# Kernel optimization log

Measured on AMD Instinct MI355X. Metric: run time of the kernel, lower is better.

Reference implementation:

```python
import jax, jax.numpy as jnp
import numpy as np

B, S, V, E, H, MAX_OOVS = 32, 1024, 32000, 256, 512, 12
D2 = 2 * H + 100          # encoder feature dim after binary concat
IN = E + D2               # GRU input size


def setup_inputs() -> dict:
    key = jax.random.key(0)
    ks = jax.random.split(key, 18)
    sc = 0.02
    return {
        "input_idx": jax.random.randint(ks[0], (B,), 0, V),
        "encoded": jax.random.normal(ks[1], (B, S, 2 * H), jnp.float32),
        "encoded_idx": jax.random.randint(ks[2], (B, S), 0, V + MAX_OOVS),
        "prev_state": jax.random.normal(ks[3], (B, H), jnp.float32),
        "weighted": jax.random.normal(ks[4], (B, 1, D2), jnp.float32),
        "binary_vectors": jax.random.uniform(ks[5], (B, S, 1), jnp.float32),
        "order": 1,
        "embed_table": jax.random.normal(ks[6], (V, E), jnp.float32) * sc,
        "W_ih": jax.random.normal(ks[7], (3 * H, IN), jnp.float32) * sc,
        "b_ih": jax.random.normal(ks[8], (3 * H,), jnp.float32) * sc,
        "W_hh": jax.random.normal(ks[9], (3 * H, H), jnp.float32) * sc,
        "b_hh": jax.random.normal(ks[10], (3 * H,), jnp.float32) * sc,
        "Wo_w": jax.random.normal(ks[11], (V, H), jnp.float32) * sc,
        "Wo_b": jax.random.normal(ks[12], (V,), jnp.float32) * sc,
        "Wc_w": jax.random.normal(ks[13], (H, D2), jnp.float32) * sc,
        "Wc_b": jax.random.normal(ks[14], (H,), jnp.float32) * sc,
        "Ws_w": jax.random.normal(ks[15], (H, D2), jnp.float32) * sc,
        "Ws_b": jax.random.normal(ks[16], (H,), jnp.float32) * sc,
    }


def _gru_step(x, h, W_ih, b_ih, W_hh, b_hh):
    # torch nn.GRU single-step math
    gi = x @ W_ih.T + b_ih
    gh = h @ W_hh.T + b_hh
    i_r, i_z, i_n = jnp.split(gi, 3, axis=1)
    h_r, h_z, h_n = jnp.split(gh, 3, axis=1)
    r = jax.nn.sigmoid(i_r + h_r)
    z = jax.nn.sigmoid(i_z + h_z)
    n = jnp.tanh(i_n + r * h_n)
    return (1.0 - z) * n + z * h


def reference(input_idx, encoded, encoded_idx, prev_state, weighted,
              binary_vectors, order, embed_table, W_ih, b_ih, W_hh, b_hh,
              Wo_w, Wo_b, Wc_w, Wc_b, Ws_w, Ws_b):
    b, s = encoded.shape[0], encoded.shape[1]
    vocab = Wo_w.shape[0]
    # concat binary feature expanded to 100 channels -> (b, s, 2H+100)
    bin100 = jnp.broadcast_to(binary_vectors, (b, s, 100))
    enc = jnp.concatenate([encoded, bin100], axis=2)

    if order == 0:
        prev_state = enc[:, -1] @ Ws_w.T + Ws_b
        weighted = jnp.zeros((b, 1, enc.shape[2]), enc.dtype)

    emb = embed_table[input_idx][:, None, :]          # (b,1,E)
    x = jnp.concatenate([emb, weighted], axis=2)[:, 0]  # (b, IN)
    state = _gru_step(x, prev_state, W_ih, b_ih, W_hh, b_hh)  # (b,H)

    score_g = state @ Wo_w.T + Wo_b                   # (b, V)
    sc = jnp.tanh(enc @ Wc_w.T + Wc_b)                # (b, s, H)
    score_c = jnp.tanh(jnp.einsum('bsh,bh->bs', sc, state))
    score_c = score_c + jnp.where(encoded_idx == 0, -1000.0, 0.0).astype(score_c.dtype)

    probs = jax.nn.softmax(jnp.concatenate([score_g, score_c], axis=1), axis=1)
    prob_g = probs[:, :vocab]
    prob_c = probs[:, vocab:]
    prob_c_given = prob_c / jnp.sum(prob_c)           # faithful: scalar sum over all elems

    oovs = jnp.full((b, MAX_OOVS), 1e-4, probs.dtype)
    prob_g = jnp.concatenate([prob_g, oovs], axis=1)  # (b, V+OOV)

    # scatter-add copy probs into vocab space (same math as one_hot + bmm)
    rows = jnp.arange(b)[:, None]
    prob_c_to_g = jnp.zeros((b, vocab + MAX_OOVS), probs.dtype).at[rows, encoded_idx].add(prob_c)
    out = (prob_g + prob_c_to_g)[:, None, :]          # (b,1,V+OOV)

    idx_from = (encoded_idx == input_idx[:, None]).astype(probs.dtype)
    ssum = idx_from.sum(axis=1, keepdims=True)
    idx_from = jnp.where(ssum > 1, idx_from / ssum, idx_from)

    attn = prob_c_given * idx_from                    # (b, s)
    weighted_out = jnp.einsum('bs,bsd->bd', attn, enc)[:, None, :]
    return out, state, weighted_out
```

## Files before the change

### kernel.cpp

```cpp
#include <hip/hip_runtime.h>

#define B_   32
#define S_   1024
#define V_   32000
#define E_   256
#define H_   512
#define D2_  1124
#define IN_  1380
#define INP_ 1408
#define G3_  1536
#define VO_  32012

typedef __bf16 bf16x8 __attribute__((ext_vector_type(8)));
typedef float  f32x4  __attribute__((ext_vector_type(4)));

static __device__ __forceinline__ unsigned short f2bf(float f) {
    union { float f; unsigned int u; } v; v.f = f;
    unsigned int u = v.u;
    unsigned int r = (u + 0x7FFFu + ((u >> 16) & 1u)) >> 16;
    return (unsigned short)r;
}

static __device__ __forceinline__ unsigned int pkbf(unsigned int a, unsigned int b) {
    return ((a + 0x8000u) >> 16) | ((b + 0x8000u) & 0xffff0000u);
}

static __device__ __forceinline__ float tanh_fast(float x) {
    float e = __builtin_amdgcn_exp2f(x * 2.8853901817f);
    return 1.0f - 2.0f * __builtin_amdgcn_rcpf(e + 1.0f);
}

__global__ void k_prep(const int* order, const int* input_idx, const float* embed,
                       const float* weighted, const float* prev,
                       const float* encoded, const float* bin,
                       const float* Ws_w, const float* Ws_b,
                       float* x, float* prev_eff) {
    int b = blockIdx.x, t = threadIdx.x;
    int ord = order[0];
    const float* emb = embed + (size_t)input_idx[b] * E_;
    for (int d = t; d < INP_; d += 256) {
        float v;
        if (d < E_)       v = emb[d];
        else if (d < IN_) v = ord ? weighted[b * D2_ + (d - E_)] : 0.0f;
        else              v = 0.0f;
        x[b * INP_ + d] = v;
    }
    if (ord) {
        for (int i = t; i < H_; i += 256) prev_eff[b * H_ + i] = prev[b * H_ + i];
    } else {
        const float* encrow = encoded + ((size_t)(b * S_ + (S_ - 1))) * 1024;
        float bv = bin[b * S_ + (S_ - 1)];
        for (int h = t; h < H_; h += 256) {
            float acc = Ws_b[h];
            const float* wr = Ws_w + (size_t)h * D2_;
            for (int d = 0; d < 1024; d++) acc += encrow[d] * wr[d];
            for (int d = 1024; d < D2_; d++) acc += bv * wr[d];
            prev_eff[b * H_ + h] = acc;
        }
    }
}

__global__ void k_pack_wc(const float* Wc_w, unsigned short* bpack) {
    int idx = blockIdx.x * 256 + threadIdx.x;
    int j = idx & 7, lane = (idx >> 3) & 63, ht = (idx >> 9) & 31, kt = idx >> 14;
    int h = ht * 16 + (lane & 15);
    int k = kt * 32 + (lane >> 4) * 8 + j;
    float v = (k < D2_) ? Wc_w[(size_t)h * D2_ + k] : 0.0f;
    bpack[idx] = f2bf(v);
}

__global__ void k_gi(const float* x, const float* W_ih, const float* b_ih, float* gi) {
    extern __shared__ float smemF[];
    int t = threadIdx.x;
    int bh = blockIdx.x & 1;
    int hq = blockIdx.x >> 1;
    const float4* xg = (const float4*)(x + (size_t)bh * 16 * INP_);
    float4* xl4 = (float4*)smemF;
    for (int j = t; j < 16 * INP_ / 4; j += 256) xl4[j] = xg[j];
    __syncthreads();
    int w = t >> 6, l = t & 63;
    int h3 = hq * 4 + w;
    const float* wr = W_ih + (size_t)h3 * IN_;
    float4 wv[6];
#pragma unroll
    for (int i = 0; i < 6; i++) {
        int k = 4 * l + 256 * i;
        if (k + 3 < IN_) wv[i] = *(const float4*)(wr + k);
        else {
            float a0 = (k     < IN_) ? wr[k]     : 0.f;
            float a1 = (k + 1 < IN_) ? wr[k + 1] : 0.f;
            float a2 = (k + 2 < IN_) ? wr[k + 2] : 0.f;
            float a3 = (k + 3 < IN_) ? wr[k + 3] : 0.f;
            wv[i] = make_float4(a0, a1, a2, a3);
        }
    }
    float bias = b_ih[h3];
    for (int bb = 0; bb < 16; bb++) {
        const float4* xr = xl4 + bb * (INP_ / 4);
        float p = 0.f;
#pragma unroll
        for (int i = 0; i < 6; i++) {
            float4 xv = xr[l + 64 * i];
            p += wv[i].x * xv.x + wv[i].y * xv.y + wv[i].z * xv.z + wv[i].w * xv.w;
        }
#pragma unroll
        for (int off = 32; off >= 1; off >>= 1) p += __shfl_xor(p, off, 64);
        if (l == 0) gi[(bh * 16 + bb) * G3_ + h3] = p + bias;
    }
}

__global__ void k_gh(const float* prev_eff, const float* W_hh, const float* b_hh, float* gh) {
    extern __shared__ float smemF[];
    int t = threadIdx.x;
    const float4* pg = (const float4*)prev_eff;
    float4* pl4 = (float4*)smemF;
    for (int j = t; j < B_ * H_ / 4; j += 256) pl4[j] = pg[j];
    __syncthreads();
    int w = t >> 6, l = t & 63;
    int h3 = blockIdx.x * 4 + w;
    const float* wr = W_hh + (size_t)h3 * H_;
    float4 w0 = *(const float4*)(wr + 4 * l);
    float4 w1 = *(const float4*)(wr + 256 + 4 * l);
    float bias = b_hh[h3];
    for (int bb = 0; bb < B_; bb++) {
        const float* pr = smemF + bb * H_;
        float4 s0 = *(const float4*)(pr + 4 * l);
        float4 s1 = *(const float4*)(pr + 256 + 4 * l);
        float p = w0.x * s0.x + w0.y * s0.y + w0.z * s0.z + w0.w * s0.w
                + w1.x * s1.x + w1.y * s1.y + w1.z * s1.z + w1.w * s1.w;
#pragma unroll
        for (int off = 32; off >= 1; off >>= 1) p += __shfl_xor(p, off, 64);
        if (l == 0) gh[bb * G3_ + h3] = p + bias;
    }
}

__global__ void k_gate(const float* gi, const float* gh, const float* prev_eff,
                       float* state, float* out_state) {
    int idx = blockIdx.x * 256 + threadIdx.x;
    int b = idx >> 9, h = idx & 511;
    float ir = gi[b * G3_ + h],           hr = gh[b * G3_ + h];
    float iz = gi[b * G3_ + H_ + h],      hz = gh[b * G3_ + H_ + h];
    float in_ = gi[b * G3_ + 2 * H_ + h], hn = gh[b * G3_ + 2 * H_ + h];
    float r = 1.0f / (1.0f + expf(-(ir + hr)));
    float z = 1.0f / (1.0f + expf(-(iz + hz)));
    float n = tanhf(in_ + r * hn);
    float st = (1.0f - z) * n + z * prev_eff[idx];
    state[idx] = st;
    out_state[idx] = st;
}

__global__ void __launch_bounds__(256) k_scoreg(const float* state, const float* Wo_w,
                                                const float* Wo_b, float* scoreg) {
    __shared__ unsigned short Abf[32 * 520];
    int t = threadIdx.x;
    {
        int m = t & 31, g = t >> 5;
        const float4* src = (const float4*)(state + m * 512 + g * 64);
        unsigned short* dst = &Abf[m * 520 + g * 64];
#pragma unroll
        for (int i = 0; i < 16; i++) {
            float4 v = src[i];
            ushort4 p; p.x = f2bf(v.x); p.y = f2bf(v.y); p.z = f2bf(v.z); p.w = f2bf(v.w);
            *(ushort4*)(dst + i * 4) = p;
        }
    }
    __syncthreads();
    int w = t >> 6, l = t & 63;
    int q = l >> 4, m16 = l & 15;
    int n = blockIdx.x * 64 + w * 16 + m16;
    const uint4* wrow = (const uint4*)(Wo_w + (size_t)n * 512 + q * 8);
    f32x4 acc0 = {0.f, 0.f, 0.f, 0.f}, acc1 = {0.f, 0.f, 0.f, 0.f};
#pragma unroll
    for (int kt = 0; kt < 16; kt++) {
        uint4 w0 = wrow[kt * 8];
        uint4 w1 = wrow[kt * 8 + 1];
        int4 pb;
        pb.x = (int)pkbf(w0.x, w0.y); pb.y = (int)pkbf(w0.z, w0.w);
        pb.z = (int)pkbf(w1.x, w1.y); pb.w = (int)pkbf(w1.z, w1.w);
        bf16x8 bv = *(bf16x8*)&pb;
        bf16x8 a0 = *(const bf16x8*)&Abf[m16 * 520 + kt * 32 + q * 8];
        bf16x8 a1 = *(const bf16x8*)&Abf[(16 + m16) * 520 + kt * 32 + q * 8];
        acc0 = __builtin_amdgcn_mfma_f32_16x16x32_bf16(a0, bv, acc0, 0, 0, 0);
        acc1 = __builtin_amdgcn_mfma_f32_16x16x32_bf16(a1, bv, acc1, 0, 0, 0);
    }
    float wb = Wo_b[n];
#pragma unroll
    for (int r = 0; r < 4; r++) {
        scoreg[(q * 4 + r) * V_ + n]        = acc0[r] + wb;
        scoreg[(16 + q * 4 + r) * V_ + n]   = acc1[r] + wb;
    }
}

__global__ void __launch_bounds__(512, 4) k_sc(
    const float* encoded, const float* bin, const unsigned short* bpack,
    const float* Wc_b, const float* state, const int* enc_idx, float* scorec) {
    __shared__ unsigned short Ab[2][64 * 136];
    __shared__ float partL[8][64];
    int t = threadIdx.x;
    int b  = blockIdx.x >> 4;
    int s0 = (blockIdx.x & 15) << 6;
    int w = t >> 6, l = t & 63;
    int q = l >> 4, m = l & 15;

    int r = t >> 3, kg = t & 7;
    const float* encbase = encoded + ((size_t)(b * S_ + s0 + r)) * 1024 + kg * 16;
    float binf = bin[b * S_ + s0 + r];
    unsigned short* dst0 = &Ab[0][r * 136 + kg * 16];
    unsigned short* dst1 = &Ab[1][r * 136 + kg * 16];

    f32x4 acc[4][4];
#pragma unroll
    for (int i = 0; i < 4; i++)
#pragma unroll
        for (int j = 0; j < 4; j++) { acc[i][j][0]=0.f; acc[i][j][1]=0.f; acc[i][j][2]=0.f; acc[i][j][3]=0.f; }

    float4 ap[4];
#pragma unroll
    for (int j = 0; j < 4; j++) ap[j] = *(const float4*)(encbase + j * 4);

    for (int s = 0; s < 9; s++) {
        unsigned short* dst = (s & 1) ? dst1 : dst0;
        if (s < 8) {
#pragma unroll
            for (int j = 0; j < 4; j++) {
                ushort4 p;
                p.x = f2bf(ap[j].x); p.y = f2bf(ap[j].y);
                p.z = f2bf(ap[j].z); p.w = f2bf(ap[j].w);
                *(ushort4*)(dst + j * 4) = p;
            }
        } else {
#pragma unroll
            for (int j = 0; j < 4; j++) {
                int kb = kg * 16 + j * 4;
                ushort4 p;
                p.x = f2bf(kb     < 100 ? binf : 0.f);
                p.y = f2bf(kb + 1 < 100 ? binf : 0.f);
                p.z = f2bf(kb + 2 < 100 ? binf : 0.f);
                p.w = f2bf(kb + 3 < 100 ? binf : 0.f);
                *(ushort4*)(dst + j * 4) = p;
            }
        }
        __syncthreads();
        if (s < 7) {
#pragma unroll
            for (int j = 0; j < 4; j++) ap[j] = *(const float4*)(encbase + (s + 1) * 128 + j * 4);
        }
        const unsigned short* abase = &Ab[s & 1][m * 136 + q * 8];
#pragma unroll
        for (int sub = 0; sub < 4; sub++) {
            int kt = s * 4 + sub;
            bf16x8 bv[4], av[4];
#pragma unroll
            for (int jj = 0; jj < 4; jj++)
                bv[jj] = *(const bf16x8*)&bpack[(((size_t)kt * 32 + (w * 4 + jj)) * 64 + l) * 8];
#pragma unroll
            for (int st = 0; st < 4; st++)
                av[st] = *(const bf16x8*)(abase + st * 16 * 136 + sub * 32);
#pragma unroll
            for (int st = 0; st < 4; st++)
#pragma unroll
                for (int jj = 0; jj < 4; jj++)
                    acc[st][jj] = __builtin_amdgcn_mfma_f32_16x16x32_bf16(av[st], bv[jj], acc[st][jj], 0, 0, 0);
        }
        __syncthreads();
    }

    float hb[4], hs[4];
#pragma unroll
    for (int jj = 0; jj < 4; jj++) {
        int h = (w * 4 + jj) * 16 + m;
        hb[jj] = Wc_b[h];
        hs[jj] = state[b * H_ + h];
    }
#pragma unroll
    for (int st = 0; st < 4; st++) {
#pragma unroll
        for (int rr = 0; rr < 4; rr++) {
            float val = 0.f;
#pragma unroll
            for (int jj = 0; jj < 4; jj++)
                val += tanh_fast(acc[st][jj][rr] + hb[jj]) * hs[jj];
            val += __shfl_xor(val, 1, 64);
            val += __shfl_xor(val, 2, 64);
            val += __shfl_xor(val, 4, 64);
            val += __shfl_xor(val, 8, 64);
            if (m == 0) partL[w][st * 16 + q * 4 + rr] = val;
        }
    }
    __syncthreads();
    if (t < 64) {
        float tot = 0.f;
#pragma unroll
        for (int ww = 0; ww < 8; ww++) tot += partL[ww][t];
        int s = s0 + t;
        int ei = enc_idx[b * S_ + s];
        scorec[b * S_ + s] = tanh_fast(tot) + (ei == 0 ? -1000.0f : 0.0f);
    }
}

__global__ void k_exp(float* scoreg, float* scorec, float* partA, float* partC) {
    int blk = blockIdx.x;
    int b = blk / 17, c = blk % 17;
    int t = threadIdx.x;
    float sa = 0.f;
    if (c < 16) {
        int base = b * V_ + c * 2000;
        for (int i = t; i < 2000; i += 256) {
            float e = __expf(scoreg[base + i]);
            scoreg[base + i] = e;
            sa += e;
        }
    } else {
        int base = b * 1024;
        for (int i = t; i < 1024; i += 256) {
            float e = __expf(scorec[base + i]);
            scorec[base + i] = e;
            sa += e;
        }
    }
#pragma unroll
    for (int off = 32; off >= 1; off >>= 1) sa += __shfl_xor(sa, off, 64);
    __shared__ float rA[4];
    int w = t >> 6, l = t & 63;
    if (l == 0) rA[w] = sa;
    __syncthreads();
    if (t == 0) {
        float tot = rA[0] + rA[1] + rA[2] + rA[3];
        partA[blk] = tot;
        if (c == 16) partC[b] = tot;
    }
}

__global__ void k_combine(const float* partA, const float* partC, float* rowinv, float* invgc,
                          int* cnt, int* list, const int* enc_idx, const int* input_idx) {
    __shared__ float rs[32], rc[32];
    int t = threadIdx.x;
    if (t < 32) {
        float a = 0.f;
        for (int j = 0; j < 17; j++) a += partA[t * 17 + j];
        rs[t] = a; rc[t] = partC[t];
        rowinv[t] = 1.0f / a;
        cnt[t] = 0;
    }
    __syncthreads();
    if (t == 0) {
        float g = 0.f;
        for (int b = 0; b < 32; b++) g += rc[b] / rs[b];
        invgc[0] = 1.0f / g;
    }
    for (int i = t; i < B_ * S_; i += 512) {
        int b = i >> 10;
        if (enc_idx[i] == input_idx[b]) {
            int p = atomicAdd(&cnt[b], 1);
            list[b * S_ + p] = i & 1023;
        }
    }
}

__global__ void k_write(const float* scoreg, const float* scorec, const float* rowinv,
                        float* out, float* probc) {
    int idx = blockIdx.x * 256 + threadIdx.x;
    if (idx < B_ * V_) {
        int b = idx / V_, v = idx - b * V_;
        out[b * VO_ + v] = scoreg[idx] * rowinv[b];
    } else if (idx < B_ * V_ + B_ * S_) {
        int j = idx - B_ * V_;
        int b = j >> 10;
        probc[j] = scorec[j] * rowinv[b];
    } else {
        int j = idx - B_ * V_ - B_ * S_;
        if (j < B_ * 12) {
            int b = j / 12;
            out[b * VO_ + V_ + (j - b * 12)] = 0.0001f;
        }
    }
}

__global__ void k_scatter(const float* probc, const int* enc_idx, float* out) {
    int idx = blockIdx.x * 256 + threadIdx.x;
    int b = idx >> 10;
    atomicAdd(&out[b * VO_ + enc_idx[idx]], probc[idx]);
}

__global__ void k_wo(const float* probc, const int* list, const int* cnt, const float* invgc,
                     const float* encoded, const float* bin, float* out2) {
    int b = blockIdx.x, t = threadIdx.x;
    __shared__ float aL[1024];
    __shared__ int   sL[1024];
    int n = cnt[b];
    float scale = invgc[0] * (n > 1 ? 1.0f / (float)n : 1.0f);
    for (int i = t; i < n; i += 256) {
        int s = list[b * S_ + i];
        sL[i] = s;
        aL[i] = probc[b * S_ + s] * scale;
    }
    __syncthreads();
    for (int d = t; d < D2_; d += 256) {
        float acc = 0.f;
        for (int i = 0; i < n; i++) {
            int s = sL[i];
            float ev = (d < 1024) ? encoded[((size_t)(b * S_ + s)) * 1024 + d] : bin[b * S_ + s];
            acc += aL[i] * ev;
        }
        out2[b * D2_ + d] = acc;
    }
}

extern "C" void kernel_launch(void* const* d_in, const int* in_sizes, int n_in,
                              void* d_out, int out_size, void* d_ws, size_t ws_size,
                              hipStream_t stream) {
    const int*   input_idx = (const int*)d_in[0];
    const float* encoded   = (const float*)d_in[1];
    const int*   enc_idx   = (const int*)d_in[2];
    const float* prev      = (const float*)d_in[3];
    const float* weighted  = (const float*)d_in[4];
    const float* bin       = (const float*)d_in[5];
    const int*   order     = (const int*)d_in[6];
    const float* embed     = (const float*)d_in[7];
    const float* W_ih      = (const float*)d_in[8];
    const float* b_ih      = (const float*)d_in[9];
    const float* W_hh      = (const float*)d_in[10];
    const float* b_hh      = (const float*)d_in[11];
    const float* Wo_w      = (const float*)d_in[12];
    const float* Wo_b      = (const float*)d_in[13];
    const float* Wc_w      = (const float*)d_in[14];
    const float* Wc_b      = (const float*)d_in[15];
    const float* Ws_w      = (const float*)d_in[16];
    const float* Ws_b      = (const float*)d_in[17];

    float* out  = (float*)d_out;
    float* out1 = out + B_ * VO_;
    float* out2 = out1 + B_ * H_;

    float* ws_f     = (float*)d_ws;
    float* w_state  = ws_f;
    float* w_prev   = ws_f + 16384;
    float* w_x      = ws_f + 68736;
    float* w_gi     = ws_f + 113792;
    float* w_gh     = ws_f + 162944;
    float* w_scoreg = ws_f + 212096;
    float* w_scorec = ws_f + 1236096;
    float* w_probc  = ws_f + 1268864;
    float* w_partA  = ws_f + 1301632;
    float* w_partC  = ws_f + 1302176;
    float* w_rowinv = ws_f + 1302208;
    float* w_invgc  = ws_f + 1302240;
    int*   w_cnt    = (int*)(ws_f + 1302248);
    int*   w_list   = w_cnt + 32;
    unsigned short* w_bpack = (unsigned short*)(ws_f + 1335048);

    k_prep<<<32, 256, 0, stream>>>(order, input_idx, embed, weighted, prev,
                                   encoded, bin, Ws_w, Ws_b, w_x, w_prev);
    k_pack_wc<<<2304, 256, 0, stream>>>(Wc_w, w_bpack);
    k_gi<<<768, 256, 16 * INP_ * sizeof(float), stream>>>(w_x, W_ih, b_ih, w_gi);
    k_gh<<<384, 256, B_ * H_ * sizeof(float), stream>>>(w_prev, W_hh, b_hh, w_gh);
    k_gate<<<64, 256, 0, stream>>>(w_gi, w_gh, w_prev, w_state, out1);
    k_scoreg<<<500, 256, 0, stream>>>(w_state, Wo_w, Wo_b, w_scoreg);
    k_sc<<<512, 512, 0, stream>>>(encoded, bin, w_bpack, Wc_b, w_state, enc_idx, w_scorec);
    k_exp<<<544, 256, 0, stream>>>(w_scoreg, w_scorec, w_partA, w_partC);
    k_combine<<<1, 512, 0, stream>>>(w_partA, w_partC, w_rowinv, w_invgc, w_cnt, w_list, enc_idx, input_idx);
    k_write<<<4130, 256, 0, stream>>>(w_scoreg, w_scorec, w_rowinv, out, w_probc);
    k_scatter<<<128, 256, 0, stream>>>(w_probc, enc_idx, out);
    k_wo<<<32, 256, 0, stream>>>(w_probc, w_list, w_cnt, w_invgc, encoded, bin, out2);
}
```

Before: 439.9 us.

## Split k_sc over H halves with atomic reduction and fuse Wc packing into prep

```diff
diff --git a/kernel.cpp b/kernel.cpp
--- a/kernel.cpp
+++ b/kernel.cpp
@@ -10,6 +10,7 @@
 #define INP_ 1408
 #define G3_  1536
 #define VO_  32012
+#define NKT_ 36
 
 typedef __bf16 bf16x8 __attribute__((ext_vector_type(8)));
 typedef float  f32x4  __attribute__((ext_vector_type(4)));
@@ -33,9 +34,20 @@
 __global__ void k_prep(const int* order, const int* input_idx, const float* embed,
                        const float* weighted, const float* prev,
                        const float* encoded, const float* bin,
-                       const float* Ws_w, const float* Ws_b,
-                       float* x, float* prev_eff) {
-    int b = blockIdx.x, t = threadIdx.x;
+                       const float* Ws_w, const float* Ws_b, const float* Wc_w,
+                       float* x, float* prev_eff, float* scorecP, unsigned short* bpack) {
+    int t = threadIdx.x;
+    if (blockIdx.x >= 32) {
+        int idx = (blockIdx.x - 32) * 256 + t;
+        int j = idx & 7, lane = (idx >> 3) & 63, ht = (idx >> 9) & 31, kt = idx >> 14;
+        int h = ht * 16 + (lane & 15);
+        int k = kt * 32 + (lane >> 4) * 8 + j;
+        float v = (k < D2_) ? Wc_w[(size_t)h * D2_ + k] : 0.0f;
+        bpack[idx] = f2bf(v);
+        return;
+    }
+    int b = blockIdx.x;
+    for (int i = t; i < S_; i += 256) scorecP[b * S_ + i] = 0.0f;
     int ord = order[0];
     const float* emb = embed + (size_t)input_idx[b] * E_;
     for (int d = t; d < INP_; d += 256) {
@@ -58,15 +70,6 @@
             prev_eff[b * H_ + h] = acc;
         }
     }
-}
-
-__global__ void k_pack_wc(const float* Wc_w, unsigned short* bpack) {
-    int idx = blockIdx.x * 256 + threadIdx.x;
-    int j = idx & 7, lane = (idx >> 3) & 63, ht = (idx >> 9) & 31, kt = idx >> 14;
-    int h = ht * 16 + (lane & 15);
-    int k = kt * 32 + (lane >> 4) * 8 + j;
-    float v = (k < D2_) ? Wc_w[(size_t)h * D2_ + k] : 0.0f;
-    bpack[idx] = f2bf(v);
 }
 
 __global__ void k_gi(const float* x, const float* W_ih, const float* b_ih, float* gi) {
@@ -191,22 +194,21 @@
     }
 }
 
-__global__ void __launch_bounds__(512, 4) k_sc(
+__global__ void __launch_bounds__(256) k_sc(
     const float* encoded, const float* bin, const unsigned short* bpack,
-    const float* Wc_b, const float* state, const int* enc_idx, float* scorec) {
-    __shared__ unsigned short Ab[2][64 * 136];
-    __shared__ float partL[8][64];
-    int t = threadIdx.x;
-    int b  = blockIdx.x >> 4;
-    int s0 = (blockIdx.x & 15) << 6;
+    const float* Wc_b, const float* state, float* scorecP) {
+    __shared__ unsigned short Albf[64 * 40];
+    __shared__ float partL[4][64];
+    int t = threadIdx.x;
+    int b  = blockIdx.x >> 5;
+    int s0 = ((blockIdx.x >> 1) & 15) << 6;
+    int hh = blockIdx.x & 1;
     int w = t >> 6, l = t & 63;
     int q = l >> 4, m = l & 15;
 
-    int r = t >> 3, kg = t & 7;
-    const float* encbase = encoded + ((size_t)(b * S_ + s0 + r)) * 1024 + kg * 16;
+    int r = t >> 2, kq = t & 3;
+    const float* encrow = encoded + ((size_t)(b * S_ + s0 + r)) * 1024 + kq * 8;
     float binf = bin[b * S_ + s0 + r];
-    unsigned short* dst0 = &Ab[0][r * 136 + kg * 16];
-    unsigned short* dst1 = &Ab[1][r * 136 + kg * 16];
 
     f32x4 acc[4][4];
 #pragma unroll
@@ -214,61 +216,52 @@
 #pragma unroll
         for (int j = 0; j < 4; j++) { acc[i][j][0]=0.f; acc[i][j][1]=0.f; acc[i][j][2]=0.f; acc[i][j][3]=0.f; }
 
-    float4 ap[4];
-#pragma unroll
-    for (int j = 0; j < 4; j++) ap[j] = *(const float4*)(encbase + j * 4);
-
-    for (int s = 0; s < 9; s++) {
-        unsigned short* dst = (s & 1) ? dst1 : dst0;
-        if (s < 8) {
-#pragma unroll
-            for (int j = 0; j < 4; j++) {
-                ushort4 p;
-                p.x = f2bf(ap[j].x); p.y = f2bf(ap[j].y);
-                p.z = f2bf(ap[j].z); p.w = f2bf(ap[j].w);
-                *(ushort4*)(dst + j * 4) = p;
-            }
+    float4 n0 = *(const float4*)(encrow);
+    float4 n1 = *(const float4*)(encrow + 4);
+    for (int kt = 0; kt < NKT_; kt++) {
+        ushort4 p0, p1;
+        if (kt < 32) {
+            p0.x = f2bf(n0.x); p0.y = f2bf(n0.y); p0.z = f2bf(n0.z); p0.w = f2bf(n0.w);
+            p1.x = f2bf(n1.x); p1.y = f2bf(n1.y); p1.z = f2bf(n1.z); p1.w = f2bf(n1.w);
         } else {
-#pragma unroll
-            for (int j = 0; j < 4; j++) {
-                int kb = kg * 16 + j * 4;
-                ushort4 p;
-                p.x = f2bf(kb     < 100 ? binf : 0.f);
-                p.y = f2bf(kb + 1 < 100 ? binf : 0.f);
-                p.z = f2bf(kb + 2 < 100 ? binf : 0.f);
-                p.w = f2bf(kb + 3 < 100 ? binf : 0.f);
-                *(ushort4*)(dst + j * 4) = p;
-            }
-        }
+            int kb = kt * 32 + kq * 8;
+            p0.x = f2bf(kb     < D2_ ? binf : 0.f);
+            p0.y = f2bf(kb + 1 < D2_ ? binf : 0.f);
+            p0.z = f2bf(kb + 2 < D2_ ? binf : 0.f);
+            p0.w = f2bf(kb + 3 < D2_ ? binf : 0.f);
+            p1.x = f2bf(kb + 4 < D2_ ? binf : 0.f);
+            p1.y = f2bf(kb + 5 < D2_ ? binf : 0.f);
+            p1.z = f2bf(kb + 6 < D2_ ? binf : 0.f);
+            p1.w = f2bf(kb + 7 < D2_ ? binf : 0.f);
+        }
+        *(ushort4*)&Albf[r * 40 + kq * 8]     = p0;
+        *(ushort4*)&Albf[r * 40 + kq * 8 + 4] = p1;
         __syncthreads();
-        if (s < 7) {
-#pragma unroll
-            for (int j = 0; j < 4; j++) ap[j] = *(const float4*)(encbase + (s + 1) * 128 + j * 4);
-        }
-        const unsigned short* abase = &Ab[s & 1][m * 136 + q * 8];
-#pragma unroll
-        for (int sub = 0; sub < 4; sub++) {
-            int kt = s * 4 + sub;
-            bf16x8 bv[4], av[4];
+        if (kt + 1 < 32) {
+            n0 = *(const float4*)(encrow + (kt + 1) * 32);
+            n1 = *(const float4*)(encrow + (kt + 1) * 32 + 4);
+        }
+        bf16x8 av[4], bv[4];
+#pragma unroll
+        for (int st = 0; st < 4; st++)
+            av[st] = *(const bf16x8*)&Albf[(st * 16 + m) * 40 + q * 8];
+#pragma unroll
+        for (int jj = 0; jj < 4; jj++) {
+            int ht = hh * 16 + w * 4 + jj;
+            bv[jj] = *(const bf16x8*)&bpack[(((size_t)kt * 32 + ht) * 64 + l) * 8];
+        }
+#pragma unroll
+        for (int st = 0; st < 4; st++)
 #pragma unroll
             for (int jj = 0; jj < 4; jj++)
-                bv[jj] = *(const bf16x8*)&bpack[(((size_t)kt * 32 + (w * 4 + jj)) * 64 + l) * 8];
-#pragma unroll
-            for (int st = 0; st < 4; st++)
-                av[st] = *(const bf16x8*)(abase + st * 16 * 136 + sub * 32);
-#pragma unroll
-            for (int st = 0; st < 4; st++)
-#pragma unroll
-                for (int jj = 0; jj < 4; jj++)
-                    acc[st][jj] = __builtin_amdgcn_mfma_f32_16x16x32_bf16(av[st], bv[jj], acc[st][jj], 0, 0, 0);
-        }
+                acc[st][jj] = __builtin_amdgcn_mfma_f32_16x16x32_bf16(av[st], bv[jj], acc[st][jj], 0, 0, 0);
         __syncthreads();
     }
 
     float hb[4], hs[4];
 #pragma unroll
     for (int jj = 0; jj < 4; jj++) {
-        int h = (w * 4 + jj) * 16 + m;
+        int h = (hh * 16 + w * 4 + jj) * 16 + m;
         hb[jj] = Wc_b[h];
         hs[jj] = state[b * H_ + h];
     }
@@ -289,16 +282,13 @@
     }
     __syncthreads();
     if (t < 64) {
-        float tot = 0.f;
-#pragma unroll
-        for (int ww = 0; ww < 8; ww++) tot += partL[ww][t];
-        int s = s0 + t;
-        int ei = enc_idx[b * S_ + s];
-        scorec[b * S_ + s] = tanh_fast(tot) + (ei == 0 ? -1000.0f : 0.0f);
-    }
-}
-
-__global__ void k_exp(float* scoreg, float* scorec, float* partA, float* partC) {
+        float tot = partL[0][t] + partL[1][t] + partL[2][t] + partL[3][t];
+        atomicAdd(&scorecP[b * S_ + s0 + t], tot);
+    }
+}
+
+__global__ void k_exp(float* scoreg, float* scorec, const int* enc_idx,
+                      float* partA, float* partC) {
     int blk = blockIdx.x;
     int b = blk / 17, c = blk % 17;
     int t = threadIdx.x;
@@ -313,7 +303,9 @@
     } else {
         int base = b * 1024;
         for (int i = t; i < 1024; i += 256) {
-            float e = __expf(scorec[base + i]);
+            float v = scorec[base + i];
+            float s = tanh_fast(v) + (enc_idx[base + i] == 0 ? -1000.0f : 0.0f);
+            float e = __expf(s);
             scorec[base + i] = e;
             sa += e;
         }
@@ -449,15 +441,15 @@
     int*   w_list   = w_cnt + 32;
     unsigned short* w_bpack = (unsigned short*)(ws_f + 1335048);
 
-    k_prep<<<32, 256, 0, stream>>>(order, input_idx, embed, weighted, prev,
-                                   encoded, bin, Ws_w, Ws_b, w_x, w_prev);
-    k_pack_wc<<<2304, 256, 0, stream>>>(Wc_w, w_bpack);
+    k_prep<<<2336, 256, 0, stream>>>(order, input_idx, embed, weighted, prev,
+                                     encoded, bin, Ws_w, Ws_b, Wc_w,
+                                     w_x, w_prev, w_scorec, w_bpack);
     k_gi<<<768, 256, 16 * INP_ * sizeof(float), stream>>>(w_x, W_ih, b_ih, w_gi);
     k_gh<<<384, 256, B_ * H_ * sizeof(float), stream>>>(w_prev, W_hh, b_hh, w_gh);
     k_gate<<<64, 256, 0, stream>>>(w_gi, w_gh, w_prev, w_state, out1);
     k_scoreg<<<500, 256, 0, stream>>>(w_state, Wo_w, Wo_b, w_scoreg);
-    k_sc<<<512, 512, 0, stream>>>(encoded, bin, w_bpack, Wc_b, w_state, enc_idx, w_scorec);
-    k_exp<<<544, 256, 0, stream>>>(w_scoreg, w_scorec, w_partA, w_partC);
+    k_sc<<<1024, 256, 0, stream>>>(encoded, bin, w_bpack, Wc_b, w_state, w_scorec);
+    k_exp<<<544, 256, 0, stream>>>(w_scoreg, w_scorec, enc_idx, w_partA, w_partC);
     k_combine<<<1, 512, 0, stream>>>(w_partA, w_partC, w_rowinv, w_invgc, w_cnt, w_list, enc_idx, input_idx);
     k_write<<<4130, 256, 0, stream>>>(w_scoreg, w_scorec, w_rowinv, out, w_probc);
     k_scatter<<<128, 256, 0, stream>>>(w_probc, enc_idx, out);
```

Result: no change. 447.6 us (+1.7%).
